# Optimization experiments

Measured on AMD Instinct MI355X. Metric: run time of the kernel, lower is better.

The kernel has to match this reference:

```python
import jax, jax.numpy as jnp
import numpy as np

B, S, D = 1, 2048, 1024
L, H, NH = 256, 1024, 16  # latent_dim, hidden_dim, num_heads
HD = H // NH
EPS = 1e-6


def rmsnorm(x, g):
    return x * jax.lax.rsqrt(jnp.mean(x * x, axis=-1, keepdims=True) + EPS) * g


def setup_inputs() -> dict:
    key = jax.random.key(0)
    ks = jax.random.split(key, 16)
    def w(k, shape, fan_in):
        return jax.random.normal(k, shape, jnp.float32) / np.sqrt(fan_in)
    return {
        "x": jax.random.normal(ks[0], (B, S, D), jnp.float32),
        "g1": jnp.ones((D,), jnp.float32),
        "Wq": w(ks[1], (D, H), D), "bq": jnp.zeros((H,), jnp.float32),
        "Wdown": w(ks[2], (D, L), D), "bdown": jnp.zeros((L,), jnp.float32),
        "Wk": w(ks[3], (L, H), L), "bk": jnp.zeros((H,), jnp.float32),
        "Wv": w(ks[4], (L, H), L), "bv": jnp.zeros((H,), jnp.float32),
        "Wo": w(ks[5], (H, D), H), "bo": jnp.zeros((D,), jnp.float32),
        "g2": jnp.ones((D,), jnp.float32),
        "W1": w(ks[6], (D, 4 * D), D), "b1": jnp.zeros((4 * D,), jnp.float32),
        "W2": w(ks[7], (4 * D, D), 4 * D), "b2": jnp.zeros((D,), jnp.float32),
    }


def reference(x, g1, Wq, bq, Wdown, bdown, Wk, bk, Wv, bv, Wo, bo, g2, W1, b1, W2, b2):
    stream = x
    # RMSNorm -> MLA (low-rank latent KV attention, causal)
    h = rmsnorm(x, g1)
    q = (h @ Wq + bq).reshape(B, S, NH, HD)
    c = h @ Wdown + bdown                       # [B,S,L] compressed KV latent
    k = (c @ Wk + bk).reshape(B, S, NH, HD)
    v = (c @ Wv + bv).reshape(B, S, NH, HD)
    scores = jnp.einsum("bqhd,bkhd->bhqk", q, k) / np.sqrt(HD)
    causal = jnp.tril(jnp.ones((S, S), bool))
    scores = jnp.where(causal, scores, jnp.finfo(scores.dtype).min)
    attn = jax.nn.softmax(scores, axis=-1)
    o = jnp.einsum("bhqk,bkhd->bqhd", attn, v).reshape(B, S, H)
    stream = (o @ Wo + bo) + stream
    # RMSNorm -> FFN (D -> 4D -> D, activation on every layer incl. last)
    h = rmsnorm(stream, g2)
    h = jax.nn.silu(h @ W1 + b1)
    h = jax.nn.silu(h @ W2 + b2)
    return h + stream
```

## Files before the change

### kernel.cpp

```cpp
#include <hip/hip_runtime.h>

typedef __bf16 bf16x8 __attribute__((ext_vector_type(8)));
typedef float  f32x4  __attribute__((ext_vector_type(4)));

static __device__ __forceinline__ ushort f2bf(float f) {
    union { float f; unsigned u; } a; a.f = f;
    unsigned r = a.u + 0x7FFFu + ((a.u >> 16) & 1u);
    return (ushort)(r >> 16);
}
static __device__ __forceinline__ ushort f2bf_hw(float f) {
    __bf16 b = (__bf16)f;
    return __builtin_bit_cast(ushort, b);
}
static __device__ __forceinline__ float bf2f(ushort u) {
    return __builtin_bit_cast(float, (unsigned)u << 16);
}

#define TS  2048
#define TD  1024
#define TL  256
#define TH  1024
#define TNH 16
#define THD 64
#define TDF 4096
#define ATT_CE 0.18033688f
#define NSPLIT 4

#define GLD_LDS(gp, lp) \
    __builtin_amdgcn_global_load_lds( \
        (const __attribute__((address_space(1))) unsigned int*)(gp), \
        (__attribute__((address_space(3))) unsigned int*)(lp), 16, 0, 0)

__global__ __launch_bounds__(256) void transpose_to_bf16(
    const float* __restrict__ in, ushort* __restrict__ out, int K, int N)
{
    __shared__ float tile[32][33];
    const int k0 = blockIdx.x * 32, n0 = blockIdx.y * 32;
    const int tx = threadIdx.x, ty = threadIdx.y;
#pragma unroll
    for (int i = ty; i < 32; i += 8)
        tile[i][tx] = in[(size_t)(k0 + i) * N + n0 + tx];
    __syncthreads();
#pragma unroll
    for (int i = ty; i < 32; i += 8)
        out[(size_t)(n0 + i) * K + k0 + tx] = f2bf(tile[tx][i]);
}

__global__ __launch_bounds__(256) void concat_bias_kernel(
    const float* __restrict__ a, const float* __restrict__ b,
    float* __restrict__ o, int n)
{
    const int i = blockIdx.x * 256 + threadIdx.x;
    o[i] = (i < n) ? a[i] : b[i - n];
}

__global__ __launch_bounds__(256) void rmsnorm_kernel(
    const float* __restrict__ x, const float* __restrict__ g,
    ushort* __restrict__ out, int D)
{
    const int row = blockIdx.x;
    const int tid = threadIdx.x;
    const float4 v = ((const float4*)(x + (size_t)row * D))[tid];
    float ss = v.x * v.x + v.y * v.y + v.z * v.z + v.w * v.w;
#pragma unroll
    for (int off = 32; off > 0; off >>= 1) ss += __shfl_down(ss, off);
    __shared__ float sums[4];
    if ((tid & 63) == 0) sums[tid >> 6] = ss;
    __syncthreads();
    const float tot = sums[0] + sums[1] + sums[2] + sums[3];
    const float scale = rsqrtf(tot / (float)D + 1e-6f);
    const float4 gv = ((const float4*)g)[tid];
    ushort4 o;
    o.x = f2bf(v.x * scale * gv.x);
    o.y = f2bf(v.y * scale * gv.y);
    o.z = f2bf(v.z * scale * gv.z);
    o.w = f2bf(v.w * scale * gv.w);
    *(ushort4*)(out + (size_t)row * D + tid * 4) = o;
}

template <int EPI, int BM, int BN, int BKH>
__global__ __launch_bounds__(256) void gemm_bf16_kernel(
    const ushort* __restrict__ A, const ushort* __restrict__ BT,
    const float* __restrict__ bias, const float* __restrict__ resid,
    void* __restrict__ outp, int M, int N, int K)
{
    constexpr int WM = BM / 2, WN = BN / 2;
    constexpr int MT = WM / 16, NT = WN / 16;
    constexpr int NLA = BM / 64, NLB = BN / 64;
    __shared__ alignas(16) ushort As[2][BKH][BM * 32];
    __shared__ alignas(16) ushort Bs[2][BKH][BN * 32];
    const int bm = blockIdx.y * BM, bn = blockIdx.x * BN;
    const int tid = threadIdx.x;
    const int lane = tid & 63, wave = tid >> 6;
    const int wr = (wave >> 1) * WM, wc = (wave & 1) * WN;
    const int l15 = lane & 15, l4 = lane >> 4;

    f32x4 acc[MT][NT] = {};

    const int grow = wave * 16 + (lane >> 2);
    const int gcol = (lane & 3) * 8;
    const ushort* Ag = A + (size_t)(bm + grow) * K + gcol;
    const ushort* Bg = BT + (size_t)(bn + grow) * K + gcol;

    auto stage = [&](int buf, int k0) {
#pragma unroll
        for (int h = 0; h < BKH; ++h) {
#pragma unroll
            for (int i = 0; i < NLA; ++i)
                GLD_LDS(Ag + (size_t)(i * 64) * K + k0 + h * 32,
                        &As[buf][h][(i * 64 + wave * 16) * 32]);
#pragma unroll
            for (int i = 0; i < NLB; ++i)
                GLD_LDS(Bg + (size_t)(i * 64) * K + k0 + h * 32,
                        &Bs[buf][h][(i * 64 + wave * 16) * 32]);
        }
    };

    stage(0, 0);
    asm volatile("s_waitcnt vmcnt(0)" ::: "memory");
    __syncthreads();

    const int nsteps = K / (32 * BKH);
    for (int t = 0; t < nsteps; ++t) {
        const int cur = t & 1;
        if (t + 1 < nsteps) stage(cur ^ 1, (t + 1) * 32 * BKH);

#pragma unroll
        for (int h = 0; h < BKH; ++h) {
            bf16x8 af[MT], bf[NT];
#pragma unroll
            for (int mt = 0; mt < MT; ++mt)
                af[mt] = *(const bf16x8*)&As[cur][h][(wr + mt * 16 + l15) * 32 + l4 * 8];
#pragma unroll
            for (int nt = 0; nt < NT; ++nt)
                bf[nt] = *(const bf16x8*)&Bs[cur][h][(wc + nt * 16 + l15) * 32 + l4 * 8];
#pragma unroll
            for (int mt = 0; mt < MT; ++mt)
#pragma unroll
                for (int nt = 0; nt < NT; ++nt)
                    acc[mt][nt] = __builtin_amdgcn_mfma_f32_16x16x32_bf16(
                        af[mt], bf[nt], acc[mt][nt], 0, 0, 0);
        }

        asm volatile("s_waitcnt vmcnt(0)" ::: "memory");
        __syncthreads();
    }

#pragma unroll
    for (int mt = 0; mt < MT; ++mt) {
#pragma unroll
        for (int nt = 0; nt < NT; ++nt) {
#pragma unroll
            for (int i = 0; i < 4; ++i) {
                const int row = bm + wr + mt * 16 + l4 * 4 + i;
                const int col = bn + wc + nt * 16 + l15;
                float v = acc[mt][nt][i] + bias[col];
                if constexpr (EPI == 1 || EPI == 3) v = v / (1.f + __expf(-v));
                if constexpr (EPI == 2 || EPI == 3) v += resid[(size_t)row * N + col];
                if constexpr (EPI == 0 || EPI == 1)
                    ((ushort*)outp)[(size_t)row * N + col] = f2bf(v);
                else
                    ((float*)outp)[(size_t)row * N + col] = v;
            }
        }
    }
}

__global__ __launch_bounds__(256) void mla_attn_kernel(
    const ushort* __restrict__ Q, const ushort* __restrict__ Kg,
    const ushort* __restrict__ Vg, ushort* __restrict__ OP, float* __restrict__ ML)
{
    constexpr int QSTR = 1024, KSTR = 2048;
    __shared__ alignas(16) ushort Ks[2][64 * 64];
    __shared__ alignas(16) ushort VTs[2][64 * 64];
    __shared__ alignas(16) ushort Ps[4][16 * 64];
    const int qb = (int)gridDim.x - 1 - (int)blockIdx.x;
    const int h = blockIdx.y;
    const int sp = blockIdx.z;
    const int tid = threadIdx.x, lane = tid & 63, wave = tid >> 6;
    const int l15 = lane & 15, l4 = lane >> 4;
    const int qrow0 = qb * 64 + wave * 16;
    const int myq = qrow0 + l15;

    const int ntile = qb + 1;
    const int chunk = (ntile + NSPLIT - 1) / NSPLIT;
    const int kt0 = sp * chunk;
    const int ktend = min(ntile, kt0 + chunk);

    auto swzK = [](ushort* base, int row, int colbyte) -> ushort* {
        return (ushort*)((char*)base + row * 128 + (colbyte ^ ((row & 7) << 4)));
    };
    auto swzVT = [](ushort* base, int d, int colbyte) -> ushort* {
        return (ushort*)((char*)base + d * 128 + (colbyte ^ (((d >> 3) & 7) << 4)));
    };
    auto swzP = [&](int row, int colbyte) -> ushort* {
        return (ushort*)((char*)&Ps[wave][0] + row * 128 + (colbyte ^ ((row & 7) << 4)));
    };

    bf16x8 qf[2];
#pragma unroll
    for (int ks = 0; ks < 2; ++ks)
        qf[ks] = *(const bf16x8*)&Q[(size_t)(qrow0 + l15) * QSTR + h * THD + ks * 32 + l4 * 8];

    f32x4 oacc[4] = {};
    float m_run = -1e30f, l_run = 0.f;

    const int sr = tid >> 3, sc = (tid & 7) * 8;
    const ushort* kbase = Kg + (size_t)sr * KSTR + h * THD + sc;
    const ushort* vbase = Vg + (size_t)sr * KSTR + h * THD + sc;

    uint4 kr0, kr1, vr0, vr1;
    if (kt0 < ktend) {
        {
            const size_t off = (size_t)kt0 * 64 * KSTR;
            kr0 = *(const uint4*)(kbase + off);
            kr1 = *(const uint4*)(kbase + off + (size_t)32 * KSTR);
            vr0 = *(const uint4*)(vbase + off);
            vr1 = *(const uint4*)(vbase + off + (size_t)32 * KSTR);
            *(uint4*)swzK(&Ks[0][0], sr, sc * 2) = kr0;
            *(uint4*)swzK(&Ks[0][0], sr + 32, sc * 2) = kr1;
            const ushort* p0 = (const ushort*)&vr0;
            const ushort* p1 = (const ushort*)&vr1;
#pragma unroll
            for (int j = 0; j < 8; ++j) {
                *swzVT(&VTs[0][0], sc + j, sr * 2) = p0[j];
                *swzVT(&VTs[0][0], sc + j, (sr + 32) * 2) = p1[j];
            }
        }
        if (kt0 + 1 < ktend) {
            const size_t off = (size_t)(kt0 + 1) * 64 * KSTR;
            kr0 = *(const uint4*)(kbase + off);
            kr1 = *(const uint4*)(kbase + off + (size_t)32 * KSTR);
            vr0 = *(const uint4*)(vbase + off);
            vr1 = *(const uint4*)(vbase + off + (size_t)32 * KSTR);
        }
    }

    for (int kt = kt0; kt < ktend; ++kt) {
        const int rel = kt - kt0;
        __syncthreads();
        if (kt + 1 < ktend) {
            ushort* kd = &Ks[(rel + 1) & 1][0];
            ushort* vd = &VTs[(rel + 1) & 1][0];
            *(uint4*)swzK(kd, sr, sc * 2) = kr0;
            *(uint4*)swzK(kd, sr + 32, sc * 2) = kr1;
            const ushort* p0 = (const ushort*)&vr0;
            const ushort* p1 = (const ushort*)&vr1;
#pragma unroll
            for (int j = 0; j < 8; ++j) {
                *swzVT(vd, sc + j, sr * 2) = p0[j];
                *swzVT(vd, sc + j, (sr + 32) * 2) = p1[j];
            }
            if (kt + 2 < ktend) {
                const size_t off = (size_t)(kt + 2) * 64 * KSTR;
                kr0 = *(const uint4*)(kbase + off);
                kr1 = *(const uint4*)(kbase + off + (size_t)32 * KSTR);
                vr0 = *(const uint4*)(vbase + off);
                vr1 = *(const uint4*)(vbase + off + (size_t)32 * KSTR);
            }
        }
        const ushort* kb_lds = &Ks[rel & 1][0];
        const ushort* vb_lds = &VTs[rel & 1][0];

        f32x4 s[4] = {};
        __builtin_amdgcn_s_setprio(1);
#pragma unroll
        for (int ks = 0; ks < 2; ++ks) {
#pragma unroll
            for (int nt = 0; nt < 4; ++nt) {
                const bf16x8 kf = *(const bf16x8*)swzK((ushort*)kb_lds, nt * 16 + l15, ks * 64 + l4 * 16);
                s[nt] = __builtin_amdgcn_mfma_f32_16x16x32_bf16(kf, qf[ks], s[nt], 0, 0, 0);
            }
        }
        __builtin_amdgcn_s_setprio(0);

        if (kt == qb) {
            const int kb = kt * 64;
#pragma unroll
            for (int nt = 0; nt < 4; ++nt)
#pragma unroll
                for (int i = 0; i < 4; ++i)
                    if (kb + nt * 16 + l4 * 4 + i > myq) s[nt][i] = -3.0e38f;
        }

        float mx = m_run;
#pragma unroll
        for (int nt = 0; nt < 4; ++nt)
#pragma unroll
            for (int i = 0; i < 4; ++i) mx = fmaxf(mx, s[nt][i]);
        mx = fmaxf(mx, __shfl_xor(mx, 16));
        mx = fmaxf(mx, __shfl_xor(mx, 32));
        const float alpha = exp2f((m_run - mx) * ATT_CE);
        m_run = mx;
        float ps = 0.f;
#pragma unroll
        for (int nt = 0; nt < 4; ++nt)
#pragma unroll
            for (int i = 0; i < 4; ++i) {
                const float p = exp2f((s[nt][i] - mx) * ATT_CE);
                s[nt][i] = p;
                ps += p;
            }
        ps += __shfl_xor(ps, 16);
        ps += __shfl_xor(ps, 32);
        l_run = l_run * alpha + ps;

#pragma unroll
        for (int dt = 0; dt < 4; ++dt)
#pragma unroll
            for (int i = 0; i < 4; ++i) oacc[dt][i] *= alpha;

#pragma unroll
        for (int nt = 0; nt < 4; ++nt) {
            ushort4 pk;
            pk.x = f2bf_hw(s[nt][0]); pk.y = f2bf_hw(s[nt][1]);
            pk.z = f2bf_hw(s[nt][2]); pk.w = f2bf_hw(s[nt][3]);
            *(ushort4*)swzP(l15, nt * 32 + l4 * 8) = pk;
        }

        __builtin_amdgcn_s_setprio(1);
#pragma unroll
        for (int ks = 0; ks < 2; ++ks) {
            const bf16x8 pf = *(const bf16x8*)swzP(l15, ks * 64 + l4 * 16);
#pragma unroll
            for (int dt = 0; dt < 4; ++dt) {
                const bf16x8 vf = *(const bf16x8*)swzVT((ushort*)vb_lds, dt * 16 + l15, ks * 64 + l4 * 16);
                oacc[dt] = __builtin_amdgcn_mfma_f32_16x16x32_bf16(vf, pf, oacc[dt], 0, 0, 0);
            }
        }
        __builtin_amdgcn_s_setprio(0);
    }

    ushort* op = OP + (size_t)sp * TS * TH;
#pragma unroll
    for (int dt = 0; dt < 4; ++dt) {
        ushort4 o4;
        o4.x = f2bf_hw(oacc[dt][0]); o4.y = f2bf_hw(oacc[dt][1]);
        o4.z = f2bf_hw(oacc[dt][2]); o4.w = f2bf_hw(oacc[dt][3]);
        *(ushort4*)&op[(size_t)myq * TH + h * THD + dt * 16 + l4 * 4] = o4;
    }
    if (l4 == 0) {
        float* ml = ML + (size_t)sp * TS * TNH * 2;
        ml[((size_t)myq * TNH + h) * 2 + 0] = m_run;
        ml[((size_t)myq * TNH + h) * 2 + 1] = l_run;
    }
}

__global__ __launch_bounds__(256) void attn_combine_kernel(
    const ushort* __restrict__ OP, const float* __restrict__ ML,
    ushort* __restrict__ O)
{
    const int idx = blockIdx.x * 256 + threadIdx.x;
    const int row = idx >> 8;
    const int h = (idx & 255) >> 4;
    float m[NSPLIT], l[NSPLIT];
#pragma unroll
    for (int sp = 0; sp < NSPLIT; ++sp) {
        m[sp] = ML[((size_t)sp * TS * TNH + (size_t)row * TNH + h) * 2 + 0];
        l[sp] = ML[((size_t)sp * TS * TNH + (size_t)row * TNH + h) * 2 + 1];
    }
    float M = m[0];
#pragma unroll
    for (int sp = 1; sp < NSPLIT; ++sp) M = fmaxf(M, m[sp]);
    float w[NSPLIT], den = 0.f;
#pragma unroll
    for (int sp = 0; sp < NSPLIT; ++sp) {
        w[sp] = exp2f((m[sp] - M) * ATT_CE);
        den += l[sp] * w[sp];
    }
    const float inv = 1.f / den;
    float ax = 0.f, ay = 0.f, az = 0.f, aw = 0.f;
#pragma unroll
    for (int sp = 0; sp < NSPLIT; ++sp) {
        const ushort4 u = ((const ushort4*)(OP + (size_t)sp * TS * TH))[idx];
        ax += w[sp] * bf2f(u.x);
        ay += w[sp] * bf2f(u.y);
        az += w[sp] * bf2f(u.z);
        aw += w[sp] * bf2f(u.w);
    }
    ushort4 o;
    o.x = f2bf_hw(ax * inv);
    o.y = f2bf_hw(ay * inv);
    o.z = f2bf_hw(az * inv);
    o.w = f2bf_hw(aw * inv);
    ((ushort4*)O)[idx] = o;
}

extern "C" void kernel_launch(void* const* d_in, const int* in_sizes, int n_in,
                              void* d_out, int out_size, void* d_ws, size_t ws_size,
                              hipStream_t stream)
{
    const float* x     = (const float*)d_in[0];
    const float* g1    = (const float*)d_in[1];
    const float* Wq    = (const float*)d_in[2];
    const float* bq    = (const float*)d_in[3];
    const float* Wdown = (const float*)d_in[4];
    const float* bdown = (const float*)d_in[5];
    const float* Wk    = (const float*)d_in[6];
    const float* bk    = (const float*)d_in[7];
    const float* Wv    = (const float*)d_in[8];
    const float* bv    = (const float*)d_in[9];
    const float* Wo    = (const float*)d_in[10];
    const float* bo    = (const float*)d_in[11];
    const float* g2    = (const float*)d_in[12];
    const float* W1    = (const float*)d_in[13];
    const float* b1    = (const float*)d_in[14];
    const float* W2    = (const float*)d_in[15];
    const float* b2    = (const float*)d_in[16];
    float* out = (float*)d_out;

    char* ws = (char*)d_ws;
    size_t off = 0;
    auto alloc = [&](size_t bytes) {
        void* p = ws + off;
        off += (bytes + 255) & ~(size_t)255;
        return p;
    };
    ushort* WqT    = (ushort*)alloc((size_t)TH * TD * 2);
    ushort* WdownT = (ushort*)alloc((size_t)TL * TD * 2);
    ushort* WkvT   = (ushort*)alloc((size_t)2 * TH * TL * 2);
    ushort* WoT    = (ushort*)alloc((size_t)TD * TH * 2);
    ushort* W1T    = (ushort*)alloc((size_t)TDF * TD * 2);
    ushort* W2T    = (ushort*)alloc((size_t)TD * TDF * 2);
    float*  bkv    = (float*)alloc((size_t)2 * TH * 4);
    ushort* hbuf   = (ushort*)alloc((size_t)TS * TD * 2);
    ushort* cbuf   = (ushort*)alloc((size_t)TS * TL * 2);
    ushort* qbuf   = (ushort*)alloc((size_t)TS * TH * 2);
    ushort* kvbuf  = (ushort*)alloc((size_t)TS * 2 * TH * 2);
    ushort* obuf   = (ushort*)alloc((size_t)TS * TH * 2);
    float*  strm   = (float*)alloc((size_t)TS * TD * 4);
    ushort* h2buf  = (ushort*)alloc((size_t)TS * TD * 2);
    ushort* ffn1   = (ushort*)alloc((size_t)TS * TDF * 2);
    float*  mlbuf  = (float*)alloc((size_t)NSPLIT * TS * TNH * 2 * 4);
    ushort* opart  = (ushort*)ffn1;

    const dim3 tb(32, 8);
    transpose_to_bf16<<<dim3(TD / 32, TH / 32), tb, 0, stream>>>(Wq, WqT, TD, TH);
    transpose_to_bf16<<<dim3(TD / 32, TL / 32), tb, 0, stream>>>(Wdown, WdownT, TD, TL);
    transpose_to_bf16<<<dim3(TL / 32, TH / 32), tb, 0, stream>>>(Wk, WkvT, TL, TH);
    transpose_to_bf16<<<dim3(TL / 32, TH / 32), tb, 0, stream>>>(Wv, WkvT + (size_t)TH * TL, TL, TH);
    transpose_to_bf16<<<dim3(TH / 32, TD / 32), tb, 0, stream>>>(Wo, WoT, TH, TD);
    transpose_to_bf16<<<dim3(TD / 32, TDF / 32), tb, 0, stream>>>(W1, W1T, TD, TDF);
    transpose_to_bf16<<<dim3(TDF / 32, TD / 32), tb, 0, stream>>>(W2, W2T, TDF, TD);
    concat_bias_kernel<<<(2 * TH) / 256, 256, 0, stream>>>(bk, bv, bkv, TH);

    rmsnorm_kernel<<<TS, 256, 0, stream>>>(x, g1, hbuf, TD);

    gemm_bf16_kernel<0, 64, 64, 2><<<dim3(TH / 64, TS / 64), 256, 0, stream>>>(
        hbuf, WqT, bq, nullptr, qbuf, TS, TH, TD);
    gemm_bf16_kernel<0, 64, 64, 2><<<dim3(TL / 64, TS / 64), 256, 0, stream>>>(
        hbuf, WdownT, bdown, nullptr, cbuf, TS, TL, TD);
    gemm_bf16_kernel<0, 64, 64, 2><<<dim3(2 * TH / 64, TS / 64), 256, 0, stream>>>(
        cbuf, WkvT, bkv, nullptr, kvbuf, TS, 2 * TH, TL);

    mla_attn_kernel<<<dim3(TS / 64, TNH, NSPLIT), 256, 0, stream>>>(
        qbuf, kvbuf, kvbuf + TH, opart, mlbuf);
    attn_combine_kernel<<<(TS * TH / 4) / 256, 256, 0, stream>>>(
        opart, mlbuf, obuf);

    gemm_bf16_kernel<2, 64, 64, 2><<<dim3(TD / 64, TS / 64), 256, 0, stream>>>(
        obuf, WoT, bo, x, strm, TS, TD, TH);

    rmsnorm_kernel<<<TS, 256, 0, stream>>>(strm, g2, h2buf, TD);

    gemm_bf16_kernel<1, 128, 128, 1><<<dim3(TDF / 128, TS / 128), 256, 0, stream>>>(
        h2buf, W1T, b1, nullptr, ffn1, TS, TDF, TD);
    gemm_bf16_kernel<3, 64, 64, 2><<<dim3(TD / 64, TS / 64), 256, 0, stream>>>(
        ffn1, W2T, b2, strm, out, TS, TD, TDF);
}
```

Measured before the change: 215.8 us.

## Fuse weight transposes, bias concat and first RMSNorm into one prep kernel

```diff
diff --git a/kernel.cpp b/kernel.cpp
--- a/kernel.cpp
+++ b/kernel.cpp
@@ -31,12 +31,12 @@
         (const __attribute__((address_space(1))) unsigned int*)(gp), \
         (__attribute__((address_space(3))) unsigned int*)(lp), 16, 0, 0)
 
-__global__ __launch_bounds__(256) void transpose_to_bf16(
-    const float* __restrict__ in, ushort* __restrict__ out, int K, int N)
-{
-    __shared__ float tile[32][33];
-    const int k0 = blockIdx.x * 32, n0 = blockIdx.y * 32;
-    const int tx = threadIdx.x, ty = threadIdx.y;
+__device__ __forceinline__ void transpose_body(
+    const float* __restrict__ in, ushort* __restrict__ out,
+    int K, int N, int bK, int bN, int tid, float (*tile)[33])
+{
+    const int k0 = bK * 32, n0 = bN * 32;
+    const int tx = tid & 31, ty = tid >> 5;
 #pragma unroll
     for (int i = ty; i < 32; i += 8)
         tile[i][tx] = in[(size_t)(k0 + i) * N + n0 + tx];
@@ -46,12 +46,64 @@
         out[(size_t)(n0 + i) * K + k0 + tx] = f2bf(tile[tx][i]);
 }
 
-__global__ __launch_bounds__(256) void concat_bias_kernel(
-    const float* __restrict__ a, const float* __restrict__ b,
-    float* __restrict__ o, int n)
-{
-    const int i = blockIdx.x * 256 + threadIdx.x;
-    o[i] = (i < n) ? a[i] : b[i - n];
+__global__ __launch_bounds__(256) void prep_kernel(
+    const float* __restrict__ x, const float* __restrict__ g1,
+    const float* __restrict__ Wq, const float* __restrict__ Wdown,
+    const float* __restrict__ Wk, const float* __restrict__ Wv,
+    const float* __restrict__ Wo, const float* __restrict__ W1,
+    const float* __restrict__ W2,
+    const float* __restrict__ bk, const float* __restrict__ bv,
+    ushort* __restrict__ WqT, ushort* __restrict__ WdownT,
+    ushort* __restrict__ WkvT, ushort* __restrict__ WoT,
+    ushort* __restrict__ W1T, ushort* __restrict__ W2T,
+    float* __restrict__ bkv, ushort* __restrict__ hbuf)
+{
+    __shared__ float tile[32][33];
+    __shared__ float sums[4];
+    int b = blockIdx.x;
+    const int tid = threadIdx.x;
+    if (b < 1024) {
+        transpose_body(Wq, WqT, TD, TH, b & 31, b >> 5, tid, tile);
+    } else if (b < 1280) {
+        b -= 1024;
+        transpose_body(Wdown, WdownT, TD, TL, b & 31, b >> 5, tid, tile);
+    } else if (b < 1536) {
+        b -= 1280;
+        transpose_body(Wk, WkvT, TL, TH, b & 7, b >> 3, tid, tile);
+    } else if (b < 1792) {
+        b -= 1536;
+        transpose_body(Wv, WkvT + (size_t)TH * TL, TL, TH, b & 7, b >> 3, tid, tile);
+    } else if (b < 2816) {
+        b -= 1792;
+        transpose_body(Wo, WoT, TH, TD, b & 31, b >> 5, tid, tile);
+    } else if (b < 6912) {
+        b -= 2816;
+        transpose_body(W1, W1T, TD, TDF, b & 31, b >> 5, tid, tile);
+    } else if (b < 11008) {
+        b -= 6912;
+        transpose_body(W2, W2T, TDF, TD, b & 127, b >> 7, tid, tile);
+    } else if (b < 11016) {
+        b -= 11008;
+        const int i = b * 256 + tid;
+        bkv[i] = (i < TH) ? bk[i] : bv[i - TH];
+    } else {
+        const int row = b - 11016;
+        const float4 v = ((const float4*)(x + (size_t)row * TD))[tid];
+        float ss = v.x * v.x + v.y * v.y + v.z * v.z + v.w * v.w;
+#pragma unroll
+        for (int off = 32; off > 0; off >>= 1) ss += __shfl_down(ss, off);
+        if ((tid & 63) == 0) sums[tid >> 6] = ss;
+        __syncthreads();
+        const float tot = sums[0] + sums[1] + sums[2] + sums[3];
+        const float scale = rsqrtf(tot / (float)TD + 1e-6f);
+        const float4 gv = ((const float4*)g1)[tid];
+        ushort4 o;
+        o.x = f2bf(v.x * scale * gv.x);
+        o.y = f2bf(v.y * scale * gv.y);
+        o.z = f2bf(v.z * scale * gv.z);
+        o.w = f2bf(v.w * scale * gv.w);
+        *(ushort4*)(hbuf + (size_t)row * TD + tid * 4) = o;
+    }
 }
 
 __global__ __launch_bounds__(256) void rmsnorm_kernel(
@@ -434,17 +486,9 @@
     float*  mlbuf  = (float*)alloc((size_t)NSPLIT * TS * TNH * 2 * 4);
     ushort* opart  = (ushort*)ffn1;
 
-    const dim3 tb(32, 8);
-    transpose_to_bf16<<<dim3(TD / 32, TH / 32), tb, 0, stream>>>(Wq, WqT, TD, TH);
-    transpose_to_bf16<<<dim3(TD / 32, TL / 32), tb, 0, stream>>>(Wdown, WdownT, TD, TL);
-    transpose_to_bf16<<<dim3(TL / 32, TH / 32), tb, 0, stream>>>(Wk, WkvT, TL, TH);
-    transpose_to_bf16<<<dim3(TL / 32, TH / 32), tb, 0, stream>>>(Wv, WkvT + (size_t)TH * TL, TL, TH);
-    transpose_to_bf16<<<dim3(TH / 32, TD / 32), tb, 0, stream>>>(Wo, WoT, TH, TD);
-    transpose_to_bf16<<<dim3(TD / 32, TDF / 32), tb, 0, stream>>>(W1, W1T, TD, TDF);
-    transpose_to_bf16<<<dim3(TDF / 32, TD / 32), tb, 0, stream>>>(W2, W2T, TDF, TD);
-    concat_bias_kernel<<<(2 * TH) / 256, 256, 0, stream>>>(bk, bv, bkv, TH);
-
-    rmsnorm_kernel<<<TS, 256, 0, stream>>>(x, g1, hbuf, TD);
+    prep_kernel<<<13064, 256, 0, stream>>>(
+        x, g1, Wq, Wdown, Wk, Wv, Wo, W1, W2, bk, bv,
+        WqT, WdownT, WkvT, WoT, W1T, W2T, bkv, hbuf);
 
     gemm_bf16_kernel<0, 64, 64, 2><<<dim3(TH / 64, TS / 64), 256, 0, stream>>>(
         hbuf, WqT, bq, nullptr, qbuf, TS, TH, TD);
@@ -463,7 +507,7 @@
 
     rmsnorm_kernel<<<TS, 256, 0, stream>>>(strm, g2, h2buf, TD);
 
-    gemm_bf16_kernel<1, 128, 128, 1><<<dim3(TDF / 128, TS / 128), 256, 0, stream>>>(
+    gemm_bf16_kernel<1, 64, 64, 2><<<dim3(TDF / 64, TS / 64), 256, 0, stream>>>(
         h2buf, W1T, b1, nullptr, ffn1, TS, TDF, TD);
     gemm_bf16_kernel<3, 64, 64, 2><<<dim3(TD / 64, TS / 64), 256, 0, stream>>>(
         ffn1, W2T, b2, strm, out, TS, TD, TDF);
```

Measured after the change: 198.8 us. 7.9% less time.
